# Performance work log

Measured on AMD Instinct MI355X. Metric: run time of the kernel, lower is better.

The kernel has to match this reference:

```python
import jax, jax.numpy as jnp
import numpy as np

NUM_SUBNETS = 64
IN, HID, OUT = 6, 4, 2   # hard-coded in SubNetwork(6, 4, 2)
GHID = 6                 # GatingNetwork(6, 6, num_subnets)
BATCH = 524288


def tanhshrink(x):
    return x - jnp.tanh(x)


def setup_inputs() -> dict:
    key = jax.random.key(0)
    ks = jax.random.split(key, 9)
    s = 0.5
    return {
        "x":    jax.random.normal(ks[0], (BATCH, IN), dtype=jnp.float32),
        # stacked per-subnet params: SubNetwork layer1 (6->4), layer2 (4->2)
        "W1":   jax.random.normal(ks[1], (NUM_SUBNETS, HID, IN), dtype=jnp.float32) * s,
        "b1":   jax.random.normal(ks[2], (NUM_SUBNETS, HID), dtype=jnp.float32) * s,
        "W2":   jax.random.normal(ks[3], (NUM_SUBNETS, OUT, HID), dtype=jnp.float32) * s,
        "b2":   jax.random.normal(ks[4], (NUM_SUBNETS, OUT), dtype=jnp.float32) * s,
        # gating network: 6 -> 6 -> num_subnets
        "Gw1":  jax.random.normal(ks[5], (GHID, IN), dtype=jnp.float32) * s,
        "Gb1":  jax.random.normal(ks[6], (GHID,), dtype=jnp.float32) * s,
        "Gw2":  jax.random.normal(ks[7], (NUM_SUBNETS, GHID), dtype=jnp.float32) * s,
        "Gb2":  jax.random.normal(ks[8], (NUM_SUBNETS,), dtype=jnp.float32) * s,
    }


def reference(x, W1, b1, W2, b2, Gw1, Gb1, Gw2, Gb2):
    # All subnet MLPs fused across the subnet axis s (batched over b):
    h = tanhshrink(jnp.einsum('bi,shi->bsh', x, W1) + b1)          # [B, S, HID]
    outs = jnp.tanh(jnp.einsum('bsh,soh->bso', h, W2) + b2)       # [B, S, OUT]
    # Gating MLP; Softmax(dim=0) on an unbatched vector == softmax over subnets per sample
    g = tanhshrink(jnp.einsum('bi,hi->bh', x, Gw1) + Gb1)          # [B, GHID]
    gate = jax.nn.softmax(jnp.einsum('bh,sh->bs', g, Gw2) + Gb2, axis=-1)  # [B, S]
    # gate_weights @ outputs
    return jnp.einsum('bs,bso->bo', gate, outs)                    # [B, OUT]
```

## Files before the change

### kernel.cpp

```cpp
#include <hip/hip_runtime.h>


#define NSUB 64
#define L2E  1.4426950408889634f
#define L2E2 2.8853900817779268f

typedef float v2f __attribute__((ext_vector_type(2)));

__device__ __forceinline__ v2f pk_fma(v2f a, v2f b, v2f c) {
    return __builtin_elementwise_fma(a, b, c);
}
__device__ __forceinline__ v2f sp(float s) { return v2f{s, s}; }

__device__ __forceinline__ v2f sig_u(v2f z) {
    v2f e;
    e.x = __builtin_amdgcn_exp2f(z.x);
    e.y = __builtin_amdgcn_exp2f(z.y);
    v2f ep = e + 1.0f;
    v2f u;
    u.x = __builtin_amdgcn_rcpf(ep.x);
    u.y = __builtin_amdgcn_rcpf(ep.y);
    return u;
}

__global__ void pack_kernel(const float* __restrict__ W1, const float* __restrict__ b1,
                            const float* __restrict__ W2, const float* __restrict__ b2,
                            const float* __restrict__ Gw2, const float* __restrict__ Gb2,
                            float* __restrict__ ws)
{
    int p = threadIdx.x;
    if (p >= 32) return;
    int sa = p, sb = p + 32;
    float* f = ws + p * 128;
    for (int i = 0; i < 24; ++i) { f[2*i]   = W1[sa*24+i]*L2E2;  f[2*i+1]   = W1[sb*24+i]*L2E2; }
    for (int i = 0; i < 4;  ++i) { f[48+2*i] = b1[sa*4+i]*L2E2;  f[48+2*i+1] = b1[sb*4+i]*L2E2; }
    for (int i = 0; i < 8;  ++i) { f[56+2*i] = W2[sa*8+i];       f[56+2*i+1] = W2[sb*8+i]; }
    for (int i = 0; i < 8;  ++i) { f[72+2*i] = W2[sa*8+i]*(2.0f*L2E2);
                                   f[72+2*i+1] = W2[sb*8+i]*(2.0f*L2E2); }
    for (int o = 0; o < 2; ++o) {
        float rsA = 0.f, rsB = 0.f;
        for (int j = 0; j < 4; ++j) { rsA += W2[sa*8+o*4+j]; rsB += W2[sb*8+o*4+j]; }
        f[88+2*o]   = (b2[sa*2+o] - rsA) * L2E2;
        f[88+2*o+1] = (b2[sb*2+o] - rsB) * L2E2;
    }
    for (int i = 0; i < 6;  ++i) { f[92+2*i] = Gw2[sa*6+i]*L2E;  f[92+2*i+1] = Gw2[sb*6+i]*L2E; }
    f[104] = Gb2[sa]*L2E; f[105] = Gb2[sb]*L2E;
    for (int i = 106; i < 128; ++i) f[i] = 0.f;
}

__device__ __forceinline__ void step(const v2f* __restrict__ f2,
                                     const float* __restrict__ xs,
                                     const float* __restrict__ ga,
                                     v2f& accE, v2f& accU0, v2f& accU1)
{
    v2f s0 = pk_fma(f2[0],  sp(xs[0]), f2[24]);
    v2f s1 = pk_fma(f2[6],  sp(xs[0]), f2[25]);
    v2f s2 = pk_fma(f2[12], sp(xs[0]), f2[26]);
    v2f s3 = pk_fma(f2[18], sp(xs[0]), f2[27]);
#pragma unroll
    for (int i = 1; i < 6; ++i) {
        v2f xi = sp(xs[i]);
        s0 = pk_fma(f2[i],      xi, s0);
        s1 = pk_fma(f2[6 + i],  xi, s1);
        s2 = pk_fma(f2[12 + i], xi, s2);
        s3 = pk_fma(f2[18 + i], xi, s3);
    }

    v2f u0 = sig_u(s0);
    v2f u1 = sig_u(s1);
    v2f u2 = sig_u(s2);
    v2f u3 = sig_u(s3);

    v2f q0 = pk_fma(f2[28], s0, f2[44]);
    q0 = pk_fma(f2[29], s1, q0);
    q0 = pk_fma(f2[30], s2, q0);
    q0 = pk_fma(f2[31], s3, q0);
    q0 = pk_fma(f2[36], u0, q0);
    q0 = pk_fma(f2[37], u1, q0);
    q0 = pk_fma(f2[38], u2, q0);
    q0 = pk_fma(f2[39], u3, q0);

    v2f q1 = pk_fma(f2[32], s0, f2[45]);
    q1 = pk_fma(f2[33], s1, q1);
    q1 = pk_fma(f2[34], s2, q1);
    q1 = pk_fma(f2[35], s3, q1);
    q1 = pk_fma(f2[40], u0, q1);
    q1 = pk_fma(f2[41], u1, q1);
    q1 = pk_fma(f2[42], u2, q1);
    q1 = pk_fma(f2[43], u3, q1);

    v2f uo0 = sig_u(q0);
    v2f uo1 = sig_u(q1);

    v2f la = pk_fma(f2[46], sp(ga[0]), f2[52]);
    la = pk_fma(f2[47], sp(ga[1]), la);
    la = pk_fma(f2[48], sp(ga[2]), la);
    la = pk_fma(f2[49], sp(ga[3]), la);
    la = pk_fma(f2[50], sp(ga[4]), la);
    la = pk_fma(f2[51], sp(ga[5]), la);
    v2f ea;
    ea.x = __builtin_amdgcn_exp2f(la.x);
    ea.y = __builtin_amdgcn_exp2f(la.y);

    accE  = accE + ea;
    accU0 = pk_fma(ea, uo0, accU0);
    accU1 = pk_fma(ea, uo1, accU1);
}

__global__ __launch_bounds__(256) void moe_kernel(
    const float* __restrict__ x,
    const float* __restrict__ wpack,
    const float* __restrict__ Gw1, const float* __restrict__ Gb1,
    float* __restrict__ out)
{
    long t = blockIdx.x * blockDim.x + threadIdx.x;

    const float4* xv = (const float4*)(x + t * 24);
    float4 v0 = xv[0], v1 = xv[1], v2 = xv[2], v3 = xv[3], v4 = xv[4], v5 = xv[5];
    float xs[4][6] = {
        {v0.x, v0.y, v0.z, v0.w, v1.x, v1.y},
        {v1.z, v1.w, v2.x, v2.y, v2.z, v2.w},
        {v3.x, v3.y, v3.z, v3.w, v4.x, v4.y},
        {v4.z, v4.w, v5.x, v5.y, v5.z, v5.w},
    };

    float ga[4][6];
#pragma unroll
    for (int j = 0; j < 6; ++j) {
        v2f sP = sp(Gb1[j]), sQ = sP;
#pragma unroll
        for (int i = 0; i < 6; ++i) {
            v2f w = sp(Gw1[j * 6 + i]);
            sP = pk_fma(w, v2f{xs[0][i], xs[1][i]}, sP);
            sQ = pk_fma(w, v2f{xs[2][i], xs[3][i]}, sQ);
        }
        v2f uP = sig_u(sP * L2E2);
        v2f uQ = sig_u(sQ * L2E2);
        v2f gP = pk_fma(sp(2.0f), uP, sP - 1.0f);
        v2f gQ = pk_fma(sp(2.0f), uQ, sQ - 1.0f);
        ga[0][j] = gP.x; ga[1][j] = gP.y;
        ga[2][j] = gQ.x; ga[3][j] = gQ.y;
    }

    v2f accE[4], U0[4], U1[4];
#pragma unroll
    for (int k = 0; k < 4; ++k) { accE[k] = sp(0.f); U0[k] = sp(0.f); U1[k] = sp(0.f); }

    for (int p = 0; p < 32; ++p) {
        const v2f* f2 = (const v2f*)(wpack + p * 128);
        step(f2, xs[0], ga[0], accE[0], U0[0], U1[0]);
        step(f2, xs[1], ga[1], accE[1], U0[1], U1[1]);
        step(f2, xs[2], ga[2], accE[2], U0[2], U1[2]);
        step(f2, xs[3], ga[3], accE[3], U0[3], U1[3]);
    }

    float4 r0, r1;
    {
        float E0 = accE[0].x + accE[0].y, E1 = accE[1].x + accE[1].y;
        float c0 = __builtin_amdgcn_rcpf(E0), c1 = __builtin_amdgcn_rcpf(E1);
        r0.x = fmaf(-2.0f * (U0[0].x + U0[0].y), c0, 1.0f);
        r0.y = fmaf(-2.0f * (U1[0].x + U1[0].y), c0, 1.0f);
        r0.z = fmaf(-2.0f * (U0[1].x + U0[1].y), c1, 1.0f);
        r0.w = fmaf(-2.0f * (U1[1].x + U1[1].y), c1, 1.0f);
    }
    {
        float E2 = accE[2].x + accE[2].y, E3 = accE[3].x + accE[3].y;
        float c2 = __builtin_amdgcn_rcpf(E2), c3 = __builtin_amdgcn_rcpf(E3);
        r1.x = fmaf(-2.0f * (U0[2].x + U0[2].y), c2, 1.0f);
        r1.y = fmaf(-2.0f * (U1[2].x + U1[2].y), c2, 1.0f);
        r1.z = fmaf(-2.0f * (U0[3].x + U0[3].y), c3, 1.0f);
        r1.w = fmaf(-2.0f * (U1[3].x + U1[3].y), c3, 1.0f);
    }
    float4* op = (float4*)&out[t * 8];
    op[0] = r0;
    op[1] = r1;
}

extern "C" void kernel_launch(void* const* d_in, const int* in_sizes, int n_in,
                              void* d_out, int out_size, void* d_ws, size_t ws_size,
                              hipStream_t stream) {
    const float* x   = (const float*)d_in[0];
    const float* W1  = (const float*)d_in[1];
    const float* b1  = (const float*)d_in[2];
    const float* W2  = (const float*)d_in[3];
    const float* b2  = (const float*)d_in[4];
    const float* Gw1 = (const float*)d_in[5];
    const float* Gb1 = (const float*)d_in[6];
    const float* Gw2 = (const float*)d_in[7];
    const float* Gb2 = (const float*)d_in[8];
    float* out = (float*)d_out;
    float* ws  = (float*)d_ws;

    pack_kernel<<<1, 64, 0, stream>>>(W1, b1, W2, b2, Gw2, Gb2, ws);

    const int threads = 256;
    const int blocks = (524288 / 4) / threads;
    moe_kernel<<<blocks, threads, 0, stream>>>(x, ws, Gw1, Gb1, out);
}
```

Before: 65.56 us.

## Split subnet loop across two thread halves and reduce partials via shared memory

Each block now has 512 threads: the two halves process the same samples but different halves of the 64 subnets, then combine softmax-denominator and weighted-output partial sums through shared memory before one half writes the result. This doubles the thread count to raise occupancy and latency hiding on a compute-bound, low-wave-count launch. It costs a duplicated gating MLP and input loads in both halves, a barrier, and a small LDS reduction.

```diff
diff --git a/kernel.cpp b/kernel.cpp
--- a/kernel.cpp
+++ b/kernel.cpp
@@ -107,15 +107,22 @@
     accU1 = pk_fma(ea, uo1, accU1);
 }
 
-__global__ __launch_bounds__(256) void moe_kernel(
+__global__ __launch_bounds__(512) void moe_kernel(
     const float* __restrict__ x,
     const float* __restrict__ wpack,
     const float* __restrict__ Gw1, const float* __restrict__ Gb1,
     float* __restrict__ out)
 {
-    long t = blockIdx.x * blockDim.x + threadIdx.x;
-
-    const float4* xv = (const float4*)(x + t * 24);
+    __shared__ float comb[256][13];
+
+    int tid  = threadIdx.x;
+    int q    = tid & 255;
+    int half = tid >> 8;
+    int pbase = __builtin_amdgcn_readfirstlane(half * 16);
+
+    long base = ((long)blockIdx.x * 256 + q) * 4;
+
+    const float4* xv = (const float4*)(x + base * 6);
     float4 v0 = xv[0], v1 = xv[1], v2 = xv[2], v3 = xv[3], v4 = xv[4], v5 = xv[5];
     float xs[4][6] = {
         {v0.x, v0.y, v0.z, v0.w, v1.x, v1.y},
@@ -146,7 +153,7 @@
 #pragma unroll
     for (int k = 0; k < 4; ++k) { accE[k] = sp(0.f); U0[k] = sp(0.f); U1[k] = sp(0.f); }
 
-    for (int p = 0; p < 32; ++p) {
+    for (int p = pbase; p < pbase + 16; ++p) {
         const v2f* f2 = (const v2f*)(wpack + p * 128);
         step(f2, xs[0], ga[0], accE[0], U0[0], U1[0]);
         step(f2, xs[1], ga[1], accE[1], U0[1], U1[1]);
@@ -154,26 +161,49 @@
         step(f2, xs[3], ga[3], accE[3], U0[3], U1[3]);
     }
 
-    float4 r0, r1;
-    {
-        float E0 = accE[0].x + accE[0].y, E1 = accE[1].x + accE[1].y;
-        float c0 = __builtin_amdgcn_rcpf(E0), c1 = __builtin_amdgcn_rcpf(E1);
-        r0.x = fmaf(-2.0f * (U0[0].x + U0[0].y), c0, 1.0f);
-        r0.y = fmaf(-2.0f * (U1[0].x + U1[0].y), c0, 1.0f);
-        r0.z = fmaf(-2.0f * (U0[1].x + U0[1].y), c1, 1.0f);
-        r0.w = fmaf(-2.0f * (U1[1].x + U1[1].y), c1, 1.0f);
-    }
-    {
-        float E2 = accE[2].x + accE[2].y, E3 = accE[3].x + accE[3].y;
-        float c2 = __builtin_amdgcn_rcpf(E2), c3 = __builtin_amdgcn_rcpf(E3);
-        r1.x = fmaf(-2.0f * (U0[2].x + U0[2].y), c2, 1.0f);
-        r1.y = fmaf(-2.0f * (U1[2].x + U1[2].y), c2, 1.0f);
-        r1.z = fmaf(-2.0f * (U0[3].x + U0[3].y), c3, 1.0f);
-        r1.w = fmaf(-2.0f * (U1[3].x + U1[3].y), c3, 1.0f);
-    }
-    float4* op = (float4*)&out[t * 8];
-    op[0] = r0;
-    op[1] = r1;
+    if (half) {
+#pragma unroll
+        for (int k = 0; k < 4; ++k) {
+            comb[q][k * 3 + 0] = accE[k].x + accE[k].y;
+            comb[q][k * 3 + 1] = U0[k].x + U0[k].y;
+            comb[q][k * 3 + 2] = U1[k].x + U1[k].y;
+        }
+    }
+    __syncthreads();
+    if (!half) {
+        float4 r0, r1;
+        {
+            float E0 = accE[0].x + accE[0].y + comb[q][0];
+            float A0 = U0[0].x + U0[0].y + comb[q][1];
+            float B0 = U1[0].x + U1[0].y + comb[q][2];
+            float E1 = accE[1].x + accE[1].y + comb[q][3];
+            float A1 = U0[1].x + U0[1].y + comb[q][4];
+            float B1 = U1[1].x + U1[1].y + comb[q][5];
+            float c0 = __builtin_amdgcn_rcpf(E0);
+            float c1 = __builtin_amdgcn_rcpf(E1);
+            r0.x = fmaf(-2.0f * A0, c0, 1.0f);
+            r0.y = fmaf(-2.0f * B0, c0, 1.0f);
+            r0.z = fmaf(-2.0f * A1, c1, 1.0f);
+            r0.w = fmaf(-2.0f * B1, c1, 1.0f);
+        }
+        {
+            float E2 = accE[2].x + accE[2].y + comb[q][6];
+            float A2 = U0[2].x + U0[2].y + comb[q][7];
+            float B2 = U1[2].x + U1[2].y + comb[q][8];
+            float E3 = accE[3].x + accE[3].y + comb[q][9];
+            float A3 = U0[3].x + U0[3].y + comb[q][10];
+            float B3 = U1[3].x + U1[3].y + comb[q][11];
+            float c2 = __builtin_amdgcn_rcpf(E2);
+            float c3 = __builtin_amdgcn_rcpf(E3);
+            r1.x = fmaf(-2.0f * A2, c2, 1.0f);
+            r1.y = fmaf(-2.0f * B2, c2, 1.0f);
+            r1.z = fmaf(-2.0f * A3, c3, 1.0f);
+            r1.w = fmaf(-2.0f * B3, c3, 1.0f);
+        }
+        float4* op = (float4*)&out[base * 2];
+        op[0] = r0;
+        op[1] = r1;
+    }
 }
 
 extern "C" void kernel_launch(void* const* d_in, const int* in_sizes, int n_in,
@@ -193,7 +223,7 @@
 
     pack_kernel<<<1, 64, 0, stream>>>(W1, b1, W2, b2, Gw2, Gb2, ws);
 
-    const int threads = 256;
-    const int blocks = (524288 / 4) / threads;
+    const int threads = 512;
+    const int blocks = (524288 / 4) / 256;
     moe_kernel<<<blocks, threads, 0, stream>>>(x, ws, Gw1, Gb1, out);
 }
```

Measured after the change: 98.44 us. 50.2% more time.
